# Optimization experiments

Hardware: AMD Instinct MI355X
Metric: run time of the kernel (lower is better)

The kernel has to match this reference:

```python
import jax, jax.numpy as jnp
import numpy as np

H = W = 128  # fixed by the hardcoded `127 - idx` in the original module


def _gather(x, gx, gy):
    # x: (B, H, W, C); gx, gy: (B, H, W) -> gathered (B, H, W, C)
    b = jnp.arange(x.shape[0])[:, None, None]
    return x[b, gx, gy]


def setup_inputs() -> dict:
    key = jax.random.key(0)
    k1, k2, k3 = jax.random.split(key, 3)
    B, C = 32, 64
    x1 = jax.random.normal(k1, (B, C, H, W), dtype=jnp.float32)
    x2 = jax.random.normal(k2, (B, C, H, W), dtype=jnp.float32)
    # 5 per-sample random bits: flipX, flipY, swap, flipX, flipY
    flip_bits = jax.random.randint(k3, (5, B), 0, 2, dtype=jnp.int32)
    return {"x1": x1, "x2": x2, "flip_bits": flip_bits}


def reference(x1, x2, flip_bits):
    B = x1.shape[0]
    x = jnp.concatenate([x1, x2], axis=1)            # (B, C_tot, H, W)
    x = jnp.transpose(x, (0, 2, 3, 1))               # NHWC for channel-last gather
    gx = jnp.broadcast_to(jnp.arange(H)[None, :, None], (B, H, W))
    gy = jnp.broadcast_to(jnp.arange(W)[None, None, :], (B, H, W))
    f = flip_bits[:, :, None, None].astype(bool)     # (5, B, 1, 1)
    # flipX
    x = _gather(x, jnp.where(f[0], (H - 1) - gx, gx), gy)
    # flipY
    x = _gather(x, gx, jnp.where(f[1], (W - 1) - gy, gy))
    # swap (transpose H/W indices per sample)
    x = _gather(x, jnp.where(f[2], gy, gx), jnp.where(f[2], gx, gy))
    # flipX
    x = _gather(x, jnp.where(f[3], (H - 1) - gx, gx), gy)
    # flipY
    x = _gather(x, gx, jnp.where(f[4], (W - 1) - gy, gy))
    x = jnp.transpose(x, (0, 3, 1, 2))               # back to NCHW
    c1 = x1.shape[1]
    return x[:, :c1], x[:, c1:]
```

## Files before the change

kernel.cpp:

```cpp
#include <hip/hip_runtime.h>


#define HWDIM 128
#define TILE  32
#define BCNT  32
#define CHALF 64

__global__ __launch_bounds__(256) void shuffle_aug_kernel(
    const float* __restrict__ x1,
    const float* __restrict__ x2,
    const int*   __restrict__ flips,
    float*       __restrict__ out)
{
    __shared__ float lds[TILE][TILE + 1];

    const int bid  = blockIdx.x;
    const int tile = bid & 15;
    const int ct   = (bid >> 4) & 127;
    const int b    = bid >> 11;

    const int f0 = flips[0 * BCNT + b];
    const int f1 = flips[1 * BCNT + b];
    const int f2 = flips[2 * BCNT + b];
    const int f3 = flips[3 * BCNT + b];
    const int f4 = flips[4 * BCNT + b];

    int sI = f3 ? -1 : 1, tI = f3 ? 127 : 0;
    int sJ = f4 ? -1 : 1, tJ = f4 ? 127 : 0;
    int sA, tA, sC, tC;
    if (f2) {
        sA = f0 ? -sJ : sJ;  tA = f0 ? 127 - tJ : tJ;
        sC = f1 ? -sI : sI;  tC = f1 ? 127 - tI : tI;
    } else {
        sA = f0 ? -sI : sI;  tA = f0 ? 127 - tI : tI;
        sC = f1 ? -sJ : sJ;  tC = f1 ? 127 - tJ : tJ;
    }

    const int ti = tile >> 2, tj = tile & 3;
    const int i0 = ti * TILE, j0 = tj * TILE;
    const int p0 = f2 ? j0 : i0;
    const int q0 = f2 ? i0 : j0;
    const int aMin = (sA > 0) ? (p0 + tA) : (tA - (p0 + TILE - 1));
    const int cMin = (sC > 0) ? (q0 + tC) : (tC - (q0 + TILE - 1));

    const int cLoc = ct & (CHALF - 1);
    const size_t plane = (size_t)(b * CHALF + cLoc) * (HWDIM * HWDIM);
    const float* __restrict__ src = (ct < CHALF ? x1 : x2) + plane;
    float* __restrict__ dst = out
        + (ct < CHALF ? (size_t)0 : (size_t)BCNT * CHALF * HWDIM * HWDIM)
        + plane;

    const int t   = threadIdx.x;
    const int vx  = t & 7;
    const int row = t >> 3;

    const float4 v = *reinterpret_cast<const float4*>(
        &src[(size_t)(aMin + row) * HWDIM + cMin + vx * 4]);
    lds[row][vx * 4 + 0] = v.x;
    lds[row][vx * 4 + 1] = v.y;
    lds[row][vx * 4 + 2] = v.z;
    lds[row][vx * 4 + 3] = v.w;

    __syncthreads();

    const int i = i0 + row;
    float4 o;
    {
        const int jb = j0 + vx * 4;
        const int q  = f2 ? i : 0;
        (void)q;
        float ov[4];
#pragma unroll
        for (int e = 0; e < 4; ++e) {
            const int j  = jb + e;
            const int p  = f2 ? j : i;
            const int qq = f2 ? i : j;
            const int a  = sA * p + tA;
            const int c  = sC * qq + tC;
            ov[e] = lds[a - aMin][c - cMin];
        }
        o.x = ov[0]; o.y = ov[1]; o.z = ov[2]; o.w = ov[3];
    }
    *reinterpret_cast<float4*>(&dst[(size_t)i * HWDIM + j0 + vx * 4]) = o;
}

extern "C" void kernel_launch(void* const* d_in, const int* in_sizes, int n_in,
                              void* d_out, int out_size, void* d_ws, size_t ws_size,
                              hipStream_t stream) {
    const float* x1    = (const float*)d_in[0];
    const float* x2    = (const float*)d_in[1];
    const int*   flips = (const int*)d_in[2];
    float*       out   = (float*)d_out;

    const int grid = BCNT * (2 * CHALF) * 16;
    shuffle_aug_kernel<<<grid, 256, 0, stream>>>(x1, x2, flips, out);
}
```

Baseline: 430.6 us.

## Process whole 128x128 plane per block with direct copy path for non-transposed samples

Each block now handles a full channel plane instead of a 32x32 tile. Samples without the swap flip skip shared memory and copy float4s directly from a flipped source address, reversing lanes when columns are reversed. Swapped samples stage the full 64KB plane in XOR-swizzled LDS to limit bank conflicts before transposing. The large LDS allocation caps occupancy at two blocks per CU, and the grid shrinks to 4096 blocks, which may reduce memory-level parallelism.

```diff
diff --git a/kernel.cpp b/kernel.cpp
--- a/kernel.cpp
+++ b/kernel.cpp
@@ -1,23 +1,23 @@
 #include <hip/hip_runtime.h>
 
 
-#define HWDIM 128
-#define TILE  32
-#define BCNT  32
-#define CHALF 64
+#define HWDIM  128
+#define BCNT   32
+#define CHALF  64
+#define NF4    (HWDIM * HWDIM / 4)
+#define PASSES (NF4 / 256)
 
-__global__ __launch_bounds__(256) void shuffle_aug_kernel(
+__global__ __launch_bounds__(256, 2) void shuffle_aug_kernel(
     const float* __restrict__ x1,
     const float* __restrict__ x2,
     const int*   __restrict__ flips,
     float*       __restrict__ out)
 {
-    __shared__ float lds[TILE][TILE + 1];
+    __shared__ float4 lds4[NF4];
 
-    const int bid  = blockIdx.x;
-    const int tile = bid & 15;
-    const int ct   = (bid >> 4) & 127;
-    const int b    = bid >> 11;
+    const int bid = blockIdx.x;
+    const int ct  = bid & 127;
+    const int b   = bid >> 7;
 
     const int f0 = flips[0 * BCNT + b];
     const int f1 = flips[1 * BCNT + b];
@@ -36,52 +36,59 @@
         sC = f1 ? -sJ : sJ;  tC = f1 ? 127 - tJ : tJ;
     }
 
-    const int ti = tile >> 2, tj = tile & 3;
-    const int i0 = ti * TILE, j0 = tj * TILE;
-    const int p0 = f2 ? j0 : i0;
-    const int q0 = f2 ? i0 : j0;
-    const int aMin = (sA > 0) ? (p0 + tA) : (tA - (p0 + TILE - 1));
-    const int cMin = (sC > 0) ? (q0 + tC) : (tC - (q0 + TILE - 1));
-
     const int cLoc = ct & (CHALF - 1);
     const size_t plane = (size_t)(b * CHALF + cLoc) * (HWDIM * HWDIM);
-    const float* __restrict__ src = (ct < CHALF ? x1 : x2) + plane;
-    float* __restrict__ dst = out
-        + (ct < CHALF ? (size_t)0 : (size_t)BCNT * CHALF * HWDIM * HWDIM)
-        + plane;
+    const float4* __restrict__ src4 =
+        reinterpret_cast<const float4*>(((ct < CHALF) ? x1 : x2) + plane);
+    float4* __restrict__ dst4 = reinterpret_cast<float4*>(
+        out + ((ct < CHALF) ? (size_t)0 : (size_t)BCNT * CHALF * HWDIM * HWDIM) + plane);
 
-    const int t   = threadIdx.x;
-    const int vx  = t & 7;
-    const int row = t >> 3;
+    const int t = threadIdx.x;
+    const bool revA = ((f2 ? (f0 ^ f4) : (f0 ^ f3)) != 0);
+    const bool revC = ((f2 ? (f1 ^ f3) : (f1 ^ f4)) != 0);
+    (void)sA; (void)tA; (void)sC; (void)tC;
 
-    const float4 v = *reinterpret_cast<const float4*>(
-        &src[(size_t)(aMin + row) * HWDIM + cMin + vx * 4]);
-    lds[row][vx * 4 + 0] = v.x;
-    lds[row][vx * 4 + 1] = v.y;
-    lds[row][vx * 4 + 2] = v.z;
-    lds[row][vx * 4 + 3] = v.w;
+    if (!f2) {
+#pragma unroll
+        for (int p = 0; p < PASSES; ++p) {
+            const int d   = p * 256 + t;
+            const int i   = d >> 5, jf4 = d & 31;
+            const int a   = revA ? (127 - i)  : i;
+            const int cf4 = revC ? (31 - jf4) : jf4;
+            float4 v = src4[(a << 5) | cf4];
+            if (revC) { float x = v.x; v.x = v.w; v.w = x;
+                        float y = v.y; v.y = v.z; v.z = y; }
+            dst4[d] = v;
+        }
+    } else {
+        float4 stage[PASSES];
+#pragma unroll
+        for (int p = 0; p < PASSES; ++p) stage[p] = src4[p * 256 + t];
+#pragma unroll
+        for (int p = 0; p < PASSES; ++p) {
+            const int d = p * 256 + t;
+            const int r = d >> 5, c4 = d & 31;
+            lds4[(r << 5) | (c4 ^ ((r >> 2) & 31))] = stage[p];
+        }
+        __syncthreads();
 
-    __syncthreads();
-
-    const int i = i0 + row;
-    float4 o;
-    {
-        const int jb = j0 + vx * 4;
-        const int q  = f2 ? i : 0;
-        (void)q;
-        float ov[4];
+        const float* __restrict__ ldsf = reinterpret_cast<const float*>(lds4);
 #pragma unroll
-        for (int e = 0; e < 4; ++e) {
-            const int j  = jb + e;
-            const int p  = f2 ? j : i;
-            const int qq = f2 ? i : j;
-            const int a  = sA * p + tA;
-            const int c  = sC * qq + tC;
-            ov[e] = lds[a - aMin][c - cMin];
+        for (int p = 0; p < PASSES; ++p) {
+            const int d = p * 256 + t;
+            const int i = d >> 5, jf4 = d & 31;
+            const int c  = revC ? (127 - i) : i;
+            const int ch = c >> 2, ce = c & 3;
+            float ov[4];
+#pragma unroll
+            for (int e = 0; e < 4; ++e) {
+                const int j = 4 * jf4 + e;
+                const int a = revA ? (127 - j) : j;
+                ov[e] = ldsf[(((a << 5) | (ch ^ ((a >> 2) & 31))) << 2) + ce];
+            }
+            dst4[d] = make_float4(ov[0], ov[1], ov[2], ov[3]);
         }
-        o.x = ov[0]; o.y = ov[1]; o.z = ov[2]; o.w = ov[3];
     }
-    *reinterpret_cast<float4*>(&dst[(size_t)i * HWDIM + j0 + vx * 4]) = o;
 }
 
 extern "C" void kernel_launch(void* const* d_in, const int* in_sizes, int n_in,
@@ -92,6 +99,6 @@
     const int*   flips = (const int*)d_in[2];
     float*       out   = (float*)d_out;
 
-    const int grid = BCNT * (2 * CHALF) * 16;
+    const int grid = BCNT * 2 * CHALF;
     shuffle_aug_kernel<<<grid, 256, 0, stream>>>(x1, x2, flips, out);
 }
```

New measurement: 437.5 us. Within noise of the previous version (+1.6%).
